# Performance work log

Hardware: AMD Instinct MI355X
Metric: run time of the kernel (lower is better)

## Reference

```python
import jax, jax.numpy as jnp
import numpy as np

BETA_MIN = 0.01
BETA_MAX = 0.995
EPS = 1e-6


def setup_inputs() -> dict:
    key = jax.random.key(0)
    k1, k2, k3, k4 = jax.random.split(key, 4)
    B, T, D = 16, 4096, 128
    return {
        "q": jax.random.normal(k1, (B, T, D), dtype=jnp.float32),
        "k": jax.random.normal(k2, (B, T, D), dtype=jnp.float32),
        "v": jax.random.normal(k3, (B, T, D), dtype=jnp.float32),
        "beta": jax.random.uniform(k4, (B, T, 1), dtype=jnp.float32),
        "mask": jnp.ones((B, T, 1), dtype=jnp.float32),
        "base_beta_1": jnp.asarray(2.0, dtype=jnp.float32),
        "base_beta_2": jnp.asarray(3.0, dtype=jnp.float32),
    }


def _delta_scan(q, k, v, beta, mask, base_beta_1, base_beta_2):
    B, T, D = q.shape
    phi_q = jax.nn.elu(q) + 1.0  # positive feature map
    phi_k = jax.nn.elu(k) + 1.0
    b1_base = jnp.clip(jax.nn.sigmoid(base_beta_1), BETA_MIN, BETA_MAX)
    b2_base = jnp.clip(jax.nn.sigmoid(base_beta_2), BETA_MIN, BETA_MAX)

    # time-major for scan: [T, B, ...]
    xs = (
        jnp.swapaxes(phi_q, 0, 1),
        jnp.swapaxes(phi_k, 0, 1),
        jnp.swapaxes(v, 0, 1),
        jnp.swapaxes(beta, 0, 1),
        jnp.swapaxes(mask, 0, 1),
    )

    H1 = jnp.zeros((B, D, D), dtype=q.dtype)
    H2 = jnp.zeros((B, D, D), dtype=q.dtype)
    Z1 = jnp.zeros((B, D), dtype=q.dtype)
    Z2 = jnp.zeros((B, D), dtype=q.dtype)

    def step(carry, x):
        H1, H2, Z1, Z2 = carry
        q_t, k_t, v_t, b_in_t, m_t = x  # q_t:[B,D], b_in_t/m_t:[B,1]
        b_in_t = jnp.clip(b_in_t, BETA_MIN, BETA_MAX)
        b1_t = jnp.clip(b1_base * b_in_t, BETA_MIN, BETA_MAX)  # [B,1]
        b2_t = jnp.clip(b2_base * b_in_t, BETA_MIN, BETA_MAX)
        kv = jnp.einsum('bd,be->bde', k_t, v_t) * m_t[:, :, None]  # masked outer product
        H1 = H1 * b1_t[:, :, None] + kv
        H2 = H2 * b2_t[:, :, None] + kv
        Z1 = Z1 * b1_t + k_t * m_t
        Z2 = Z2 * b2_t + k_t * m_t
        num = jnp.einsum('bd,bde->be', q_t, H1 + H2)
        den = jnp.maximum(jnp.sum(q_t * (Z1 + Z2), axis=-1, keepdims=True), EPS)
        o_t = num / den * m_t
        return (H1, H2, Z1, Z2), o_t

    _, outs = jax.lax.scan(step, (H1, H2, Z1, Z2), xs)
    return jnp.swapaxes(outs, 0, 1)  # [B, T, D]


def reference(q, k, v, beta, mask, base_beta_1, base_beta_2):
    return _delta_scan(q, k, v, beta, mask, base_beta_1, base_beta_2)
```

## Files before the change

### kernel.cpp

```cpp
#include <hip/hip_runtime.h>

#define B_ 16
#define T_ 4096
#define D_ 128
#define L_ 128
#define NC_ 32
#define CH_ (B_*NC_)
#define LDP 136

typedef __attribute__((ext_vector_type(8))) short bf16x8;
typedef __attribute__((ext_vector_type(4))) float f32x4;

__device__ __forceinline__ float clampf(float x, float lo, float hi) {
    return fminf(fmaxf(x, lo), hi);
}
__device__ __forceinline__ float phi_f(float x) {
    return x > 0.f ? x + 1.f : __expf(x);
}
__device__ __forceinline__ unsigned short bf16r(float f) {
    unsigned u = __builtin_bit_cast(unsigned, f);
    u += 0x7FFFu + ((u >> 16) & 1u);
    return (unsigned short)(u >> 16);
}
__device__ __forceinline__ float fbf(unsigned short h) {
    unsigned u = ((unsigned)h) << 16; return __builtin_bit_cast(float, u);
}
__device__ __forceinline__ unsigned pack2bf(float a, float b) {
    return (unsigned)bf16r(a) | ((unsigned)bf16r(b) << 16);
}
__device__ __forceinline__ uint4 pack8(const float* f) {
    uint4 r;
    r.x = pack2bf(f[0], f[1]); r.y = pack2bf(f[2], f[3]);
    r.z = pack2bf(f[4], f[5]); r.w = pack2bf(f[6], f[7]);
    return r;
}
__device__ __forceinline__ f32x4 zero4() { f32x4 z; z[0]=0.f; z[1]=0.f; z[2]=0.f; z[3]=0.f; return z; }

__device__ __forceinline__ int aidx(int row, int k0) {
    return (((row >> 4) * 4 + (k0 >> 5)) * 64 + ((k0 >> 3) & 3) * 16 + (row & 15)) * 8;
}

__global__ __launch_bounds__(256) void kS(
        const float* __restrict__ kk, const float* __restrict__ vv,
        const float* __restrict__ mask,
        const float* __restrict__ beta,
        const float* __restrict__ bb1, const float* __restrict__ bb2,
        unsigned short* __restrict__ phiKT, unsigned short* __restrict__ VtT,
        float* __restrict__ lg1, float* __restrict__ lg2, float* __restrict__ wexp) {
    int g = blockIdx.x;
    int ch = g >> 2, q = g & 3;
    int b = ch / NC_, c = ch % NC_;
    int tbase = b * T_ + c * L_;
    int tid = threadIdx.x;
    size_t cb = (size_t)ch * 16384;
    __shared__ float tot1s[2], tot2s[2];

    float cx1 = 0.f, cx2 = 0.f;
    int clane = tid & 63, cw = tid >> 6;
    if (q == 0 && tid < 128) {
        float b1b = clampf(1.f / (1.f + __expf(-bb1[0])), 0.01f, 0.995f);
        float b2b = clampf(1.f / (1.f + __expf(-bb2[0])), 0.01f, 0.995f);
        float be = clampf(beta[tbase + tid], 0.01f, 0.995f);
        cx1 = __logf(clampf(b1b * be, 0.01f, 0.995f));
        cx2 = __logf(clampf(b2b * be, 0.01f, 0.995f));
#pragma unroll
        for (int off = 1; off < 64; off <<= 1) {
            float y1 = __shfl_up(cx1, off);
            float y2 = __shfl_up(cx2, off);
            if (clane >= off) { cx1 += y1; cx2 += y2; }
        }
        if (clane == 63) { tot1s[cw] = cx1; tot2s[cw] = cx2; }
    }
    __syncthreads();
    if (q == 0 && tid < 128) {
        if (cw == 1) { cx1 += tot1s[0]; cx2 += tot2s[0]; }
        float tot1 = tot1s[0] + tot1s[1];
        float tot2 = tot2s[0] + tot2s[1];
        lg1[tbase + tid] = cx1;
        lg2[tbase + tid] = cx2;
        wexp[(size_t)ch * 128 + tid]                     = __expf(tot1 - cx1);
        wexp[(size_t)CH_ * 128 + (size_t)ch * 128 + tid] = __expf(tot2 - cx2);
    }

#pragma unroll
    for (int p = 0; p < 2; ++p) {
        int i = p * 256 + tid;
        int s = q * 32 + (i >> 4), d0 = (i & 15) * 8;
        const float* kp = &kk[(size_t)(tbase + s) * D_ + d0];
        float4 x0 = *(const float4*)kp, x1 = *(const float4*)(kp + 4);
        float m = mask[tbase + s];
        float pq[8] = {phi_f(x0.x)*m, phi_f(x0.y)*m, phi_f(x0.z)*m, phi_f(x0.w)*m,
                       phi_f(x1.x)*m, phi_f(x1.y)*m, phi_f(x1.z)*m, phi_f(x1.w)*m};
        *(uint4*)&phiKT[cb + aidx(s, d0)] = pack8(pq);
    }

#pragma unroll
    for (int p = 0; p < 2; ++p) {
        int i = p * 256 + tid;
        int e = q * 32 + (i & 31), s0 = (i >> 5) * 8;
        const float* vp = &vv[(size_t)(tbase + s0) * D_ + e];
        float f[8];
#pragma unroll
        for (int j = 0; j < 8; ++j)
            f[j] = vp[(size_t)j * D_];
        *(uint4*)&VtT[cb + aidx(e, s0)] = pack8(f);
    }
}

__global__ __launch_bounds__(512, 4) void kC(
        const float* __restrict__ kk, const float* __restrict__ mask,
        const unsigned short* __restrict__ VtT, const float* __restrict__ wexp,
        unsigned short* __restrict__ Cws, float* __restrict__ zc) {
    int g = blockIdx.x;
    int ch = ((g >> 4) << 3) | (g & 7);
    int st = (g >> 3) & 1;
    int b = ch / NC_, c = ch % NC_;
    int tbase = b * T_ + c * L_;
    int tid = threadIdx.x, lane = tid & 63, w = tid >> 6;
    int l15 = lane & 15, lg4 = lane >> 4;
    size_t cb = (size_t)ch * 16384;
    __shared__ unsigned short sKt[16384];

#pragma unroll
    for (int p = 0; p < 4; ++p) {
        int i = p * 512 + tid;
        int d = i & 127, s0 = (i >> 7) * 8;
        const float* kp = &kk[(size_t)(tbase + s0) * D_ + d];
        const float* mp = &mask[tbase + s0];
        float f[8];
#pragma unroll
        for (int j = 0; j < 8; ++j)
            f[j] = phi_f(kp[(size_t)j * D_]) * mp[j];
        *(uint4*)&sKt[aidx(d, s0)] = pack8(f);
    }
    __syncthreads();

    const float* wp = &wexp[(size_t)st * CH_ * 128 + (size_t)ch * 128];

    f32x4 acc[8];
#pragma unroll
    for (int n = 0; n < 8; ++n) acc[n] = zero4();
    float zp[8] = {0.f, 0.f, 0.f, 0.f, 0.f, 0.f, 0.f, 0.f};

#pragma unroll
    for (int ks = 0; ks < 4; ++ks) {
        int koff = ks * 32 + lg4 * 8;
        float wl[8];
        {
            float4 a0 = *(const float4*)&wp[koff];
            float4 a1 = *(const float4*)&wp[koff + 4];
            wl[0]=a0.x; wl[1]=a0.y; wl[2]=a0.z; wl[3]=a0.w;
            wl[4]=a1.x; wl[5]=a1.y; wl[6]=a1.z; wl[7]=a1.w;
        }
        bf16x8 as;
        {
            bf16x8 vt = *(const bf16x8*)&VtT[cb + (size_t)(((w * 4 + ks) * 64 + lane) * 8)];
#pragma unroll
            for (int j = 0; j < 8; ++j)
                as[j] = (short)bf16r(fbf((unsigned short)vt[j]) * wl[j]);
        }
        bf16x8 bb[8];
#pragma unroll
        for (int n = 0; n < 8; ++n)
            bb[n] = *(const bf16x8*)&sKt[((n * 4 + ks) * 64 + lane) * 8];
        if (w == 0) {
#pragma unroll
            for (int n = 0; n < 8; ++n)
#pragma unroll
                for (int j = 0; j < 8; ++j)
                    zp[n] += wl[j] * fbf((unsigned short)bb[n][j]);
        }
#pragma unroll
        for (int n = 0; n < 8; ++n)
            acc[n] = __builtin_amdgcn_mfma_f32_16x16x32_bf16(as, bb[n], acc[n], 0, 0, 0);
    }

    if (w == 0) {
#pragma unroll
        for (int n = 0; n < 8; ++n) {
            float z = zp[n];
            z += __shfl_xor(z, 16); z += __shfl_xor(z, 32);
            if (lg4 == 0)
                zc[((size_t)(st * B_ + b) * NC_ + c) * D_ + n * 16 + l15] = z;
        }
    }

    __syncthreads();
#pragma unroll
    for (int n = 0; n < 8; ++n)
#pragma unroll
        for (int r = 0; r < 4; ++r) {
            int e = w * 16 + lg4 * 4 + r;
            int d = n * 16 + l15;
            sKt[aidx(e, d & ~7) + (d & 7)] = bf16r(acc[n][r]);
        }
    __syncthreads();
    unsigned short* Cp = Cws + ((size_t)(st * B_ + b) * NC_ + c) * (D_ * D_);
#pragma unroll
    for (int p = 0; p < 4; ++p) {
        int i = p * 512 + tid;
        *(uint4*)&Cp[(size_t)i * 8] = *(const uint4*)&sKt[i * 8];
    }
}

__global__ void k2f(unsigned short* __restrict__ Cws, float* __restrict__ zc,
                    const float* __restrict__ lg1, const float* __restrict__ lg2) {
    int g = blockIdx.x * blockDim.x + threadIdx.x;
    if (g < 131072) {
        int st = g >> 16;
        int rem = g & 65535;
        int b = rem >> 12;
        int de = (rem & 4095) * 4;
        const float* lg = st ? lg2 : lg1;
        size_t base = ((size_t)(st * B_ + b) * NC_) * (D_ * D_) + de;
        float run0 = 0.f, run1 = 0.f, run2 = 0.f, run3 = 0.f;
#pragma unroll
        for (int c = 0; c < NC_; c++) {
            float a = __expf(lg[b * T_ + c * L_ + L_ - 1]);
            uint2 val = *(uint2*)&Cws[base + (size_t)c * (D_ * D_)];
            float t0 = fbf((unsigned short)(val.x & 0xffff)), t1 = fbf((unsigned short)(val.x >> 16));
            float t2 = fbf((unsigned short)(val.y & 0xffff)), t3 = fbf((unsigned short)(val.y >> 16));
            uint2 wv; wv.x = pack2bf(run0, run1); wv.y = pack2bf(run2, run3);
            *(uint2*)&Cws[base + (size_t)c * (D_ * D_)] = wv;
            run0 = a * run0 + t0; run1 = a * run1 + t1;
            run2 = a * run2 + t2; run3 = a * run3 + t3;
        }
    } else {
        int gz = g - 131072;
        int st = gz >> 11;
        int rem = gz & 2047;
        int b = rem >> 7;
        int d = rem & 127;
        const float* lg = st ? lg2 : lg1;
        size_t base = ((size_t)(st * B_ + b) * NC_) * D_ + d;
        float run = 0.f;
#pragma unroll
        for (int c = 0; c < NC_; c++) {
            float a = __expf(lg[b * T_ + c * L_ + L_ - 1]);
            float tmp = zc[base + (size_t)c * D_];
            zc[base + (size_t)c * D_] = run;
            run = a * run + tmp;
        }
    }
}

__global__ __launch_bounds__(512, 2) void k3_v10(
        const float* __restrict__ qq, const float* __restrict__ mask,
        const float* __restrict__ lg1, const float* __restrict__ lg2,
        const unsigned short* __restrict__ phiKT, const unsigned short* __restrict__ VtT,
        const unsigned short* __restrict__ Cws, const float* __restrict__ zc,
        float* __restrict__ out) {
    __shared__ unsigned short sQ[128 * LDP];
    __shared__ unsigned short bufP[8][16 * LDP];
    __shared__ float sOsc[128], sA1[128], sA2[128];
    int ch = blockIdx.x;
    int b = ch / NC_, c = ch % NC_;
    int tbase = b * T_ + c * L_;
    int tid = threadIdx.x, lane = tid & 63, w = tid >> 6;
    int l15 = lane & 15, lg4 = lane >> 4;
    size_t cb = (size_t)ch * 16384;
    unsigned short* sPK = &bufP[0][0];

#pragma unroll
    for (int p = 0; p < 4; ++p) {
        int i = p * 512 + tid;
        *(uint4*)&sPK[i * 8] = *(const uint4*)&phiKT[cb + (size_t)i * 8];
    }

    int trow = w * 16 + l15;
    size_t gt = (size_t)(tbase + trow);
    float lg1t = lg1[gt], lg2t = lg2[gt], mt = mask[gt];
    float a1t = __expf(lg1t), a2t = __expf(lg2t);

    bf16x8 qf[4];
#pragma unroll
    for (int ks = 0; ks < 4; ++ks) {
        int koff = ks * 32 + lg4 * 8;
        const float* qp = &qq[gt * D_ + koff];
        float4 x0 = *(const float4*)qp, x1 = *(const float4*)(qp + 4);
        float p0[8] = {phi_f(x0.x), phi_f(x0.y), phi_f(x0.z), phi_f(x0.w),
                       phi_f(x1.x), phi_f(x1.y), phi_f(x1.z), phi_f(x1.w)};
#pragma unroll
        for (int j = 0; j < 8; ++j) qf[ks][j] = (short)bf16r(p0[j]);
        *(uint4*)&sQ[trow * LDP + koff] = __builtin_bit_cast(uint4, qf[ks]);
    }

    const float* z1p = &zc[((size_t)(0 * B_ + b) * NC_ + c) * D_];
    const float* z2p = &zc[((size_t)(1 * B_ + b) * NC_ + c) * D_];
    float d1 = 0.f, d2 = 0.f;
#pragma unroll
    for (int ks = 0; ks < 4; ++ks) {
        int off = ks * 32 + lg4 * 8;
        float4 za = *(const float4*)(z1p + off), zb = *(const float4*)(z1p + off + 4);
        float4 zca = *(const float4*)(z2p + off), zcb = *(const float4*)(z2p + off + 4);
        float z1a[8] = {za.x, za.y, za.z, za.w, zb.x, zb.y, zb.z, zb.w};
        float z2a[8] = {zca.x, zca.y, zca.z, zca.w, zcb.x, zcb.y, zcb.z, zcb.w};
#pragma unroll
        for (int j = 0; j < 8; ++j) {
            float fq = fbf((unsigned short)qf[ks][j]);
            d1 += fq * z1a[j]; d2 += fq * z2a[j];
        }
    }
    d1 += __shfl_xor(d1, 16); d1 += __shfl_xor(d1, 32);
    d2 += __shfl_xor(d2, 16); d2 += __shfl_xor(d2, 32);

    __syncthreads();

    int SN = (w | 1) + 1;
    int KP = SN >> 1;
    f32x4 accs[8];
#pragma unroll
    for (int x = 0; x < 8; ++x) accs[x] = zero4();
#pragma unroll
    for (int sp = 0; sp < 4; ++sp) {
        if (sp < KP) {
            bf16x8 kf[8];
#pragma unroll
            for (int mm = 0; mm < 2; ++mm)
#pragma unroll
                for (int ks = 0; ks < 4; ++ks)
                    kf[mm * 4 + ks] = *(const bf16x8*)&sPK[((((sp * 2 + mm) * 4) + ks) * 64 + lane) * 8];
#pragma unroll
            for (int ks = 0; ks < 4; ++ks) {
                accs[sp * 2 + 0] = __builtin_amdgcn_mfma_f32_16x16x32_bf16(kf[ks],     qf[ks], accs[sp * 2 + 0], 0, 0, 0);
                accs[sp * 2 + 1] = __builtin_amdgcn_mfma_f32_16x16x32_bf16(kf[4 + ks], qf[ks], accs[sp * 2 + 1], 0, 0, 0);
            }
        }
    }
    __syncthreads();

    float rs = 0.f;
#pragma unroll
    for (int sp = 0; sp < 4; ++sp) {
        if (sp < KP) {
#pragma unroll
            for (int mm = 0; mm < 2; ++mm) {
                int s0 = (sp * 2 + mm) * 16 + lg4 * 4;
                float4 l1s = *(const float4*)&lg1[tbase + s0];
                float4 l2s = *(const float4*)&lg2[tbase + s0];
                float l1a[4] = {l1s.x, l1s.y, l1s.z, l1s.w};
                float l2a[4] = {l2s.x, l2s.y, l2s.z, l2s.w};
                float pv[4];
#pragma unroll
                for (int r = 0; r < 4; ++r) {
                    int s = s0 + r;
                    float p = 0.f;
                    if (s <= trow)
                        p = accs[sp * 2 + mm][r] * (__expf(lg1t - l1a[r]) + __expf(lg2t - l2a[r]));
                    pv[r] = p; rs += p;
                }
                uint2 dd; dd.x = pack2bf(pv[0], pv[1]); dd.y = pack2bf(pv[2], pv[3]);
                *(uint2*)&bufP[w][l15 * LDP + s0] = dd;
            }
        }
    }
    rs += __shfl_xor(rs, 16); rs += __shfl_xor(rs, 32);
    float osc = mt / fmaxf(a1t * d1 + a2t * d2 + rs, 1e-6f);
    if (lg4 == 0) {
        sOsc[trow] = osc;
        sA1[trow] = a1t;
        sA2[trow] = a2t;
    }
    __syncthreads();

    {
        int m = w;
        bf16x8 vf[4];
#pragma unroll
        for (int ks = 0; ks < 4; ++ks)
            vf[ks] = *(const bf16x8*)&VtT[cb + (size_t)(((m * 4 + ks) * 64 + lane) * 8)];

        f32x4 accO[8];
#pragma unroll
        for (int tt = 0; tt < 8; ++tt) accO[tt] = zero4();

#pragma unroll
        for (int st = 0; st < 2; ++st) {
            const unsigned short* Hp = Cws + ((size_t)(st * B_ + b) * NC_ + c) * (D_ * D_);
            bf16x8 hf[4];
#pragma unroll
            for (int ks = 0; ks < 4; ++ks)
                hf[ks] = *(const bf16x8*)&Hp[(size_t)(((m * 4 + ks) * 64 + lane) * 8)];
            f32x4 U[8];
#pragma unroll
            for (int tt = 0; tt < 8; ++tt) U[tt] = zero4();
#pragma unroll
            for (int ks = 0; ks < 4; ++ks) {
                int koff = ks * 32 + lg4 * 8;
#pragma unroll
                for (int tt = 0; tt < 8; ++tt) {
                    bf16x8 qb = *(const bf16x8*)&sQ[(tt * 16 + l15) * LDP + koff];
                    U[tt] = __builtin_amdgcn_mfma_f32_16x16x32_bf16(hf[ks], qb, U[tt], 0, 0, 0);
                }
            }
            const float* sA = st ? sA2 : sA1;
#pragma unroll
            for (int tt = 0; tt < 8; ++tt) {
                float sc = sA[tt * 16 + l15];
#pragma unroll
                for (int r = 0; r < 4; ++r) accO[tt][r] += sc * U[tt][r];
            }
        }

#pragma unroll
        for (int tt = 0; tt < 8; ++tt) {
            int KPt = ((tt | 1) + 1) >> 1;
            for (int ks = 0; ks < KPt; ++ks) {
                bf16x8 pf = *(const bf16x8*)&bufP[tt][l15 * LDP + ks * 32 + lg4 * 8];
                accO[tt] = __builtin_amdgcn_mfma_f32_16x16x32_bf16(vf[ks], pf, accO[tt], 0, 0, 0);
            }
        }

#pragma unroll
        for (int tt = 0; tt < 8; ++tt) {
            float oscr = sOsc[tt * 16 + l15];
            float4 o;
            o.x = accO[tt][0] * oscr; o.y = accO[tt][1] * oscr;
            o.z = accO[tt][2] * oscr; o.w = accO[tt][3] * oscr;
            *(float4*)&out[(size_t)(tbase + tt * 16 + l15) * D_ + m * 16 + lg4 * 4] = o;
        }
    }
}

extern "C" void kernel_launch(void* const* d_in, const int* in_sizes, int n_in,
                              void* d_out, int out_size, void* d_ws, size_t ws_size,
                              hipStream_t stream) {
    const float* q    = (const float*)d_in[0];
    const float* k    = (const float*)d_in[1];
    const float* v    = (const float*)d_in[2];
    const float* beta = (const float*)d_in[3];
    const float* mask = (const float*)d_in[4];
    const float* bb1  = (const float*)d_in[5];
    const float* bb2  = (const float*)d_in[6];
    float* out = (float*)d_out;

    size_t n_lg = (size_t)B_ * T_;
    size_t n_z  = (size_t)2 * B_ * NC_ * D_;
    size_t n_w  = (size_t)2 * CH_ * 128;
    size_t n_C  = (size_t)2 * B_ * NC_ * D_ * D_;
    size_t n_kt = (size_t)B_ * T_ * D_;
    size_t need = (2 * n_lg + n_z + n_w) * sizeof(float) + (n_C + 2 * n_kt) * sizeof(unsigned short);
    if (ws_size < need) return;

    float* lg1  = (float*)d_ws;
    float* lg2  = lg1 + n_lg;
    float* zc   = lg2 + n_lg;
    float* wexp = zc + n_z;
    unsigned short* Cws    = (unsigned short*)(wexp + n_w);
    unsigned short* phiKT  = Cws + n_C;
    unsigned short* VtT    = phiKT + n_kt;

    kS<<<4 * CH_, 256, 0, stream>>>(k, v, mask, beta, bb1, bb2, phiKT, VtT, lg1, lg2, wexp);
    kC<<<2 * CH_, 512, 0, stream>>>(k, mask, VtT, wexp, Cws, zc);
    k2f<<<528, 256, 0, stream>>>(Cws, zc, lg1, lg2);
    k3_v10<<<CH_, 512, 0, stream>>>(q, mask, lg1, lg2, phiKT, VtT, Cws, zc, out);
}
```

Baseline: 78.32 us.

## Precompute bf16 phi(q) in prep kernel and reuse bf16 phi(k) in chunk kernel

The prep kernel now also applies phi to q and writes it as bf16 into a new workspace buffer. The output kernel loads that bf16 tile into shared memory instead of reading fp32 q and applying phi itself. The chunk-state kernel reads the already-packed bf16 phi(k) buffer and transposes it in shared memory rather than re-reading fp32 k and mask. Output stores become nontemporal. The aim is less fp32 global traffic and less repeated phi work in the later kernels, at the cost of an extra bf16 write and read of q, scattered 2-byte shared stores in kC, and one more barrier in the output kernel.

```diff
diff --git a/kernel.cpp b/kernel.cpp
--- a/kernel.cpp
+++ b/kernel.cpp
@@ -41,11 +41,13 @@
 }
 
 __global__ __launch_bounds__(256) void kS(
+        const float* __restrict__ qq,
         const float* __restrict__ kk, const float* __restrict__ vv,
         const float* __restrict__ mask,
         const float* __restrict__ beta,
         const float* __restrict__ bb1, const float* __restrict__ bb2,
-        unsigned short* __restrict__ phiKT, unsigned short* __restrict__ VtT,
+        unsigned short* __restrict__ phiKT, unsigned short* __restrict__ phiQT,
+        unsigned short* __restrict__ VtT,
         float* __restrict__ lg1, float* __restrict__ lg2, float* __restrict__ wexp) {
     int g = blockIdx.x;
     int ch = g >> 2, q = g & 3;
@@ -97,6 +99,17 @@
 #pragma unroll
     for (int p = 0; p < 2; ++p) {
         int i = p * 256 + tid;
+        int s = q * 32 + (i >> 4), d0 = (i & 15) * 8;
+        const float* qp = &qq[(size_t)(tbase + s) * D_ + d0];
+        float4 x0 = *(const float4*)qp, x1 = *(const float4*)(qp + 4);
+        float pq[8] = {phi_f(x0.x), phi_f(x0.y), phi_f(x0.z), phi_f(x0.w),
+                       phi_f(x1.x), phi_f(x1.y), phi_f(x1.z), phi_f(x1.w)};
+        *(uint4*)&phiQT[cb + (size_t)(s * 128 + d0)] = pack8(pq);
+    }
+
+#pragma unroll
+    for (int p = 0; p < 2; ++p) {
+        int i = p * 256 + tid;
         int e = q * 32 + (i & 31), s0 = (i >> 5) * 8;
         const float* vp = &vv[(size_t)(tbase + s0) * D_ + e];
         float f[8];
@@ -108,14 +121,13 @@
 }
 
 __global__ __launch_bounds__(512, 4) void kC(
-        const float* __restrict__ kk, const float* __restrict__ mask,
+        const unsigned short* __restrict__ phiKT,
         const unsigned short* __restrict__ VtT, const float* __restrict__ wexp,
         unsigned short* __restrict__ Cws, float* __restrict__ zc) {
     int g = blockIdx.x;
     int ch = ((g >> 4) << 3) | (g & 7);
     int st = (g >> 3) & 1;
     int b = ch / NC_, c = ch % NC_;
-    int tbase = b * T_ + c * L_;
     int tid = threadIdx.x, lane = tid & 63, w = tid >> 6;
     int l15 = lane & 15, lg4 = lane >> 4;
     size_t cb = (size_t)ch * 16384;
@@ -123,15 +135,18 @@
 
 #pragma unroll
     for (int p = 0; p < 4; ++p) {
-        int i = p * 512 + tid;
-        int d = i & 127, s0 = (i >> 7) * 8;
-        const float* kp = &kk[(size_t)(tbase + s0) * D_ + d];
-        const float* mp = &mask[tbase + s0];
-        float f[8];
+        int o = p * 512 + tid;
+        uint4 pk = *(const uint4*)&phiKT[cb + (size_t)o * 8];
+        int l15s = o & 15, kgrp = (o >> 4) & 3, ktile = (o >> 6) & 3, stile = o >> 8;
+        int s = stile * 16 + l15s, d0 = ktile * 32 + kgrp * 8;
+        unsigned short pu[8] = {
+            (unsigned short)(pk.x & 0xffff), (unsigned short)(pk.x >> 16),
+            (unsigned short)(pk.y & 0xffff), (unsigned short)(pk.y >> 16),
+            (unsigned short)(pk.z & 0xffff), (unsigned short)(pk.z >> 16),
+            (unsigned short)(pk.w & 0xffff), (unsigned short)(pk.w >> 16)};
 #pragma unroll
         for (int j = 0; j < 8; ++j)
-            f[j] = phi_f(kp[(size_t)j * D_]) * mp[j];
-        *(uint4*)&sKt[aidx(d, s0)] = pack8(f);
+            sKt[aidx(d0 + j, s & ~7) + (s & 7)] = pu[j];
     }
     __syncthreads();
 
@@ -244,10 +259,11 @@
     }
 }
 
-__global__ __launch_bounds__(512, 2) void k3_v10(
-        const float* __restrict__ qq, const float* __restrict__ mask,
+__global__ __launch_bounds__(512, 2) void k3_v12(
+        const float* __restrict__ mask,
         const float* __restrict__ lg1, const float* __restrict__ lg2,
-        const unsigned short* __restrict__ phiKT, const unsigned short* __restrict__ VtT,
+        const unsigned short* __restrict__ phiKT, const unsigned short* __restrict__ phiQT,
+        const unsigned short* __restrict__ VtT,
         const unsigned short* __restrict__ Cws, const float* __restrict__ zc,
         float* __restrict__ out) {
     __shared__ unsigned short sQ[128 * LDP];
@@ -265,6 +281,8 @@
     for (int p = 0; p < 4; ++p) {
         int i = p * 512 + tid;
         *(uint4*)&sPK[i * 8] = *(const uint4*)&phiKT[cb + (size_t)i * 8];
+        int t = i >> 4, d0 = (i & 15) * 8;
+        *(uint4*)&sQ[t * LDP + d0] = *(const uint4*)&phiQT[cb + (size_t)i * 8];
     }
 
     int trow = w * 16 + l15;
@@ -272,18 +290,12 @@
     float lg1t = lg1[gt], lg2t = lg2[gt], mt = mask[gt];
     float a1t = __expf(lg1t), a2t = __expf(lg2t);
 
+    __syncthreads();
+
     bf16x8 qf[4];
 #pragma unroll
-    for (int ks = 0; ks < 4; ++ks) {
-        int koff = ks * 32 + lg4 * 8;
-        const float* qp = &qq[gt * D_ + koff];
-        float4 x0 = *(const float4*)qp, x1 = *(const float4*)(qp + 4);
-        float p0[8] = {phi_f(x0.x), phi_f(x0.y), phi_f(x0.z), phi_f(x0.w),
-                       phi_f(x1.x), phi_f(x1.y), phi_f(x1.z), phi_f(x1.w)};
-#pragma unroll
-        for (int j = 0; j < 8; ++j) qf[ks][j] = (short)bf16r(p0[j]);
-        *(uint4*)&sQ[trow * LDP + koff] = __builtin_bit_cast(uint4, qf[ks]);
-    }
+    for (int ks = 0; ks < 4; ++ks)
+        qf[ks] = *(const bf16x8*)&sQ[trow * LDP + ks * 32 + lg4 * 8];
 
     const float* z1p = &zc[((size_t)(0 * B_ + b) * NC_ + c) * D_];
     const float* z2p = &zc[((size_t)(1 * B_ + b) * NC_ + c) * D_];
@@ -303,8 +315,6 @@
     }
     d1 += __shfl_xor(d1, 16); d1 += __shfl_xor(d1, 32);
     d2 += __shfl_xor(d2, 16); d2 += __shfl_xor(d2, 32);
-
-    __syncthreads();
 
     int SN = (w | 1) + 1;
     int KP = SN >> 1;
@@ -414,10 +424,11 @@
 #pragma unroll
         for (int tt = 0; tt < 8; ++tt) {
             float oscr = sOsc[tt * 16 + l15];
-            float4 o;
-            o.x = accO[tt][0] * oscr; o.y = accO[tt][1] * oscr;
-            o.z = accO[tt][2] * oscr; o.w = accO[tt][3] * oscr;
-            *(float4*)&out[(size_t)(tbase + tt * 16 + l15) * D_ + m * 16 + lg4 * 4] = o;
+            f32x4 o;
+            o[0] = accO[tt][0] * oscr; o[1] = accO[tt][1] * oscr;
+            o[2] = accO[tt][2] * oscr; o[3] = accO[tt][3] * oscr;
+            f32x4* op = (f32x4*)&out[(size_t)(tbase + tt * 16 + l15) * D_ + m * 16 + lg4 * 4];
+            __builtin_nontemporal_store(o, op);
         }
     }
 }
@@ -439,7 +450,7 @@
     size_t n_w  = (size_t)2 * CH_ * 128;
     size_t n_C  = (size_t)2 * B_ * NC_ * D_ * D_;
     size_t n_kt = (size_t)B_ * T_ * D_;
-    size_t need = (2 * n_lg + n_z + n_w) * sizeof(float) + (n_C + 2 * n_kt) * sizeof(unsigned short);
+    size_t need = (2 * n_lg + n_z + n_w) * sizeof(float) + (n_C + 3 * n_kt) * sizeof(unsigned short);
     if (ws_size < need) return;
 
     float* lg1  = (float*)d_ws;
@@ -448,10 +459,11 @@
     float* wexp = zc + n_z;
     unsigned short* Cws    = (unsigned short*)(wexp + n_w);
     unsigned short* phiKT  = Cws + n_C;
-    unsigned short* VtT    = phiKT + n_kt;
-
-    kS<<<4 * CH_, 256, 0, stream>>>(k, v, mask, beta, bb1, bb2, phiKT, VtT, lg1, lg2, wexp);
-    kC<<<2 * CH_, 512, 0, stream>>>(k, mask, VtT, wexp, Cws, zc);
+    unsigned short* phiQT  = phiKT + n_kt;
+    unsigned short* VtT    = phiQT + n_kt;
+
+    kS<<<4 * CH_, 256, 0, stream>>>(q, k, v, mask, beta, bb1, bb2, phiKT, phiQT, VtT, lg1, lg2, wexp);
+    kC<<<2 * CH_, 512, 0, stream>>>(phiKT, VtT, wexp, Cws, zc);
     k2f<<<528, 256, 0, stream>>>(Cws, zc, lg1, lg2);
-    k3_v10<<<CH_, 512, 0, stream>>>(q, mask, lg1, lg2, phiKT, VtT, Cws, zc, out);
-}
+    k3_v12<<<CH_, 512, 0, stream>>>(mask, lg1, lg2, phiKT, phiQT, VtT, Cws, zc, out);
+}
```

New measurement: 80.51 us. 2.8% more time.
